# Kernel optimization log

Hardware: AMD Instinct MI355X
Metric: run time of the kernel (lower is better)

Reference implementation:

```python
import jax, jax.numpy as jnp
import numpy as np

B, NB, NS, C, HID, NP, NH = 8, 2048, 1024, 768, 3072, 1024, 6
HD = C // NH


def _ln(x, w, b):
    mu = x.mean(-1, keepdims=True)
    var = ((x - mu) ** 2).mean(-1, keepdims=True)
    return (x - mu) / jnp.sqrt(var + 1e-5) * w + b


def _gelu(z):
    return jax.nn.gelu(z, approximate=False)  # torch nn.GELU default = exact erf


def setup_inputs() -> dict:
    key = jax.random.key(0)
    ks = jax.random.split(key, 16)
    p = lambda i, shape: (jax.random.normal(ks[i], shape, jnp.float32) * 0.02)
    inp = {
        'x_b': jax.random.normal(ks[0], (B, NB, C), jnp.float32),
        'x_s': jax.random.normal(ks[1], (B, NS, C), jnp.float32),
        # token_types[0,0]=0 -> KV is computed (no stale cache), as on the first call
        'token_types': jax.random.randint(ks[2], (B, NS), 0, 2, jnp.int32).at[0, 0].set(0),
        'base_idxs': jax.random.randint(ks[3], (B, NP), -3, NB).astype(jnp.int32),
        'ln1_w': jnp.ones(C, jnp.float32), 'ln1_b': jnp.zeros(C, jnp.float32),
        'ln2_w': jnp.ones(C, jnp.float32), 'ln2_b': jnp.zeros(C, jnp.float32),
        'ln3_w': jnp.ones(C, jnp.float32), 'ln3_b': jnp.zeros(C, jnp.float32),
        'Wq': p(4, (C, C)), 'Wkv': p(5, (C, 2 * C)),
        'es_w1': p(6, (C, HID)), 'es_b1': jnp.zeros(HID, jnp.float32),
        'es_w2': p(7, (HID, C)), 'es_b2': jnp.zeros(C, jnp.float32),
        'el_w1': p(8, (C, HID)), 'el_b1': jnp.zeros(HID, jnp.float32),
        'el_w2': p(9, (HID, C)), 'el_b2': jnp.zeros(C, jnp.float32),
        'mlp_w1': p(10, (C, 4 * C)), 'mlp_b1': jnp.zeros(4 * C, jnp.float32),
        'mlp_w2': p(11, (4 * C, C)), 'mlp_b2': jnp.zeros(C, jnp.float32),
    }
    return inp


def reference(x_b, x_s, token_types, base_idxs,
              ln1_w, ln1_b, ln2_w, ln2_b, ln3_w, ln3_b,
              Wq, Wkv, es_w1, es_b1, es_w2, es_b2,
              el_w1, el_b1, el_w2, el_b2,
              mlp_w1, mlp_b1, mlp_w2, mlp_b2):
    Bn, Ns, Cd = x_s.shape
    # --- norm1/norm2 + cross-attention (q from x_s, kv from x_b) ---
    xs_n = _ln(x_s, ln1_w, ln1_b)
    xb_n = _ln(x_b, ln2_w, ln2_b)
    q = (xs_n @ Wq).reshape(Bn, Ns, NH, HD).transpose(0, 2, 1, 3)          # (B,H,Ns,hd)
    kv = (xb_n @ Wkv).reshape(Bn, -1, 2, NH, HD).transpose(2, 0, 3, 1, 4)  # (2,B,H,Nb,hd)
    k_, v_ = kv[0], kv[1]
    attn = jax.nn.softmax(jnp.einsum('bhqd,bhkd->bhqk', q, k_) * (HD ** -0.5), axis=-1)
    ctx = jnp.einsum('bhqk,bhkd->bhqd', attn, v_).transpose(0, 2, 1, 3).reshape(Bn, Ns, Cd)
    # --- 2-expert MoE MLP routed by token_types (0 -> expert_s, 1 -> expert_l) ---
    out_s = _gelu(ctx @ es_w1 + es_b1) @ es_w2 + es_b2
    out_l = _gelu(ctx @ el_w1 + el_b1) @ el_w2 + el_b2
    tt = token_types[..., None]
    moe = jnp.where(tt == 0, out_s, 0.0) + jnp.where(tt == 1, out_l, 0.0)
    x = x_s + moe
    # --- residual MLP ---
    x = x + (_gelu(_ln(x, ln3_w, ln3_b) @ mlp_w1 + mlp_b1) @ mlp_w2 + mlp_b2)
    x_norm = x / jnp.maximum(jnp.linalg.norm(x, axis=-1, keepdims=True), 1e-12)
    # --- masked-token kernel (vectorized over batch, masking replaces gather) ---
    nh = base_idxs.shape[1] // 2
    ids = base_idxs[:, :nh]
    mask = ids >= 0                                        # (B,nh)
    idc = jnp.where(mask, ids, 0)
    tokens = jnp.take_along_axis(x_b, idc[:, :, None], axis=1) * mask[..., None]
    sc = jnp.einsum('bic,bjc->bij', tokens, tokens) / jnp.sqrt(jnp.float32(Cd))
    kbias = jnp.where(mask, 0.0, -1e9)[:, None, :]
    aw = jax.nn.softmax(sc + kbias, axis=-1)
    agg = jnp.einsum('bij,bjc->bic', aw, tokens)
    cnt = mask.sum(-1)
    ksum = (agg * mask[..., None]).sum(1) / jnp.maximum(cnt, 1)[:, None]
    kn = ksum / jnp.maximum(jnp.linalg.norm(ksum, axis=-1, keepdims=True), 1e-12)
    has = (cnt > 0)[:, None]
    kernel = jnp.where(has, kn, 0.0)                        # (B,C)
    pos = jnp.where(has, (jnp.einsum('bnc,bc->bn', x_norm, kernel) + 1.0) / 2.0, 0.0)
    # --- top-k selection with data-dependent valid_k and straight-through binarize ---
    kk = Ns // 8
    topv, topi = jax.lax.top_k(pos, kk)
    cnt65 = (pos > 0.65).sum(-1)
    vk = jnp.minimum(kk, jnp.maximum(kk - 10, cnt65))
    keep = jnp.arange(kk)[None, :] < vk[:, None]
    vals = topv * keep
    sel = vals[:, :, None] * jax.nn.one_hot(topi, Ns, dtype=x.dtype)
    binary = (sel > 0.0).astype(x.dtype)
    sel = sel + jax.lax.stop_gradient(binary - sel)
    return sel, topi, pos, x, kernel[:, None, :]
```

## Files before the change

### kernel.cpp

```cpp
#include <hip/hip_runtime.h>
#include <hip/hip_bf16.h>
#include <math.h>

#define B_   8
#define NB_  2048
#define NS_  1024
#define Cc_  768
#define HID_ 3072
#define NP_  1024
#define NH_  6
#define HD_  128

__device__ __forceinline__ float gelu_exact(float v) {
  return 0.5f * v * (1.0f + erff(v * 0.7071067811865476f));
}

__device__ __forceinline__ void split3(float v, unsigned short& h,
                                       unsigned short& m, unsigned short& l) {
  unsigned hb = __float_as_uint(v) & 0xffff0000u;
  float r1 = v - __uint_as_float(hb);
  unsigned mb = __float_as_uint(r1) & 0xffff0000u;
  float r2 = r1 - __uint_as_float(mb);
  unsigned lb = __float_as_uint(r2) & 0xffff0000u;
  h = (unsigned short)(hb >> 16);
  m = (unsigned short)(mb >> 16);
  l = (unsigned short)(lb >> 16);
}

typedef short bf16x8 __attribute__((ext_vector_type(8)));
typedef float f32x4 __attribute__((ext_vector_type(4)));

#define BLOCK_REDUCE_ADD(red, tid)                                              \
  for (int off_ = 128; off_; off_ >>= 1) {                                      \
    if ((tid) < off_) red[(tid)] += red[(tid) + off_];                          \
    __syncthreads();                                                            \
  }

__global__ __launch_bounds__(256) void ln_split(
    const float* __restrict__ x, unsigned short* __restrict__ y,
    const float* __restrict__ w, const float* __restrict__ b) {
  __shared__ float red[256];
  int row = blockIdx.x, tid = threadIdx.x;
  const float* xr = x + (size_t)row * Cc_;
  float v0 = xr[tid], v1 = xr[tid + 256], v2 = xr[tid + 512];
  red[tid] = v0 + v1 + v2;
  __syncthreads();
  BLOCK_REDUCE_ADD(red, tid);
  float mu = red[0] / (float)Cc_;
  __syncthreads();
  float d0 = v0 - mu, d1 = v1 - mu, d2 = v2 - mu;
  red[tid] = d0 * d0 + d1 * d1 + d2 * d2;
  __syncthreads();
  BLOCK_REDUCE_ADD(red, tid);
  float var = red[0] / (float)Cc_;
  float rs = 1.0f / sqrtf(var + 1e-5f);
  unsigned short* yr = y + (size_t)row * 2304;
  float vals[3] = {d0 * rs * w[tid] + b[tid],
                   d1 * rs * w[tid + 256] + b[tid + 256],
                   d2 * rs * w[tid + 512] + b[tid + 512]};
#pragma unroll
  for (int t = 0; t < 3; ++t) {
    int c = tid + (t << 8);
    unsigned short h16, m16, l16;
    split3(vals[t], h16, m16, l16);
    yr[c] = h16; yr[768 + c] = m16; yr[1536 + c] = l16;
  }
}

__global__ __launch_bounds__(256) void split_kernel(
    const float* __restrict__ x, unsigned short* __restrict__ y) {
  size_t idx = (size_t)blockIdx.x * 256 + threadIdx.x;
  int c = (int)(idx % Cc_);
  int row = (int)(idx / Cc_);
  unsigned short h16, m16, l16;
  split3(x[idx], h16, m16, l16);
  unsigned short* yr = y + (size_t)row * 2304;
  yr[c] = h16; yr[768 + c] = m16; yr[1536 + c] = l16;
}

__global__ __launch_bounds__(256) void rownorm_kernel(
    const float* __restrict__ x, float* __restrict__ y) {
  __shared__ float red[256];
  int row = blockIdx.x, tid = threadIdx.x;
  const float* xr = x + (size_t)row * Cc_;
  float* yr = y + (size_t)row * Cc_;
  float v0 = xr[tid], v1 = xr[tid + 256], v2 = xr[tid + 512];
  red[tid] = v0 * v0 + v1 * v1 + v2 * v2;
  __syncthreads();
  BLOCK_REDUCE_ADD(red, tid);
  float den = fmaxf(sqrtf(red[0]), 1e-12f);
  yr[tid]       = v0 / den;
  yr[tid + 256] = v1 / den;
  yr[tid + 512] = v2 / den;
}

__global__ __launch_bounds__(256) void wconv(
    const float* __restrict__ W, unsigned short* __restrict__ out,
    int K, int N, int ldw, int ncol0) {
  int k = blockIdx.x * 256 + threadIdx.x;
  int n = blockIdx.y;
  float v = W[(size_t)k * ldw + ncol0 + n];
  unsigned short h16, m16, l16;
  split3(v, h16, m16, l16);
  size_t base = (size_t)n * 3 * K;
  out[base + k] = h16;
  out[base + K + k] = m16;
  out[base + 2 * K + k] = l16;
}

template <int EPI, bool AGATHER, bool MDEV, bool SWZ>
__global__ __launch_bounds__(256) void mgemm(
    const unsigned short* __restrict__ Ap, const unsigned short* __restrict__ Bp,
    float* __restrict__ Cf, unsigned short* __restrict__ Cs,
    const float* __restrict__ bias,
    const int* __restrict__ perm, const int* __restrict__ mdev,
    int M, int N, int K, int ldc, int Kout, int nsplit,
    long azs, long bzs, long zstride, float scale) {
  __shared__ unsigned short As[2][8192];
  __shared__ unsigned short Bs[2][8192];
  int z = blockIdx.z;
  int bx, by;
  if (SWZ) {
    int gx = gridDim.x;
    int id = blockIdx.y * gx + blockIdx.x;
    int per = (gx * gridDim.y) >> 3;
    int nid = (id & 7) * per + (id >> 3);
    bx = nid % gx; by = nid / gx;
  } else {
    bx = blockIdx.x; by = blockIdx.y;
  }
  int Me = MDEV ? mdev[0] : M;
  int m0 = by * 128, n0 = bx * 128;
  if (MDEV && m0 >= Me) return;
  const unsigned short* ApB = Ap + (size_t)z * azs;
  const unsigned short* BpB = Bp + (size_t)z * bzs;
  int tid = threadIdx.x;
  int lane = tid & 63, w = tid >> 6;
  int wr = w >> 1, wc = w & 1;
  int K3 = 3 * K;
  int tps = K >> 6;
  int KT = 6 * tps;
  int span = KT / nsplit;
  int zr = z % nsplit;
  int tt0 = zr * span, tt1 = tt0 + span;

  const unsigned short* agp[4];
  const unsigned short* bgp[4];
  int wswz[4];
#pragma unroll
  for (int p = 0; p < 4; ++p) {
    int r = (tid >> 3) + 32 * p;
    int ma = m0 + r;
    if (MDEV) ma = min(ma, Me - 1);
    if (AGATHER) ma = perm[ma];
    agp[p] = ApB + (size_t)ma * K3 + (tid & 7) * 8;
    bgp[p] = BpB + (size_t)(n0 + r) * K3 + (tid & 7) * 8;
    wswz[p] = r * 64 + (((tid & 7) ^ (r & 7)) << 3);
  }

  f32x4 acc[4][4];
  f32x4 zero4 = {0.f, 0.f, 0.f, 0.f};
#pragma unroll
  for (int i = 0; i < 4; ++i)
#pragma unroll
    for (int j = 0; j < 4; ++j) acc[i][j] = zero4;

  int kg = lane >> 4;
  int frm[4], frn[4];
#pragma unroll
  for (int f = 0; f < 4; ++f) {
    frm[f] = wr * 64 + f * 16 + (lane & 15);
    frn[f] = wc * 64 + f * 16 + (lane & 15);
  }

  bf16x8 ra[4], rb[4];
  {
    int seg = tt0 / tps, kt = tt0 - seg * tps;
    int pa = (0x210100u >> (4 * seg)) & 0xF;
    int pb = (0x012010u >> (4 * seg)) & 0xF;
    size_t ao = (size_t)(pa * K + kt * 64);
    size_t bo = (size_t)(pb * K + kt * 64);
#pragma unroll
    for (int p = 0; p < 4; ++p) {
      ra[p] = *(const bf16x8*)(agp[p] + ao);
      rb[p] = *(const bf16x8*)(bgp[p] + bo);
    }
  }

  for (int tt = tt0; tt < tt1; ++tt) {
    int cur = tt & 1;
#pragma unroll
    for (int p = 0; p < 4; ++p) {
      *(bf16x8*)&As[cur][wswz[p]] = ra[p];
      *(bf16x8*)&Bs[cur][wswz[p]] = rb[p];
    }
    if (tt + 1 < tt1) {
      int seg = (tt + 1) / tps, kt = (tt + 1) - seg * tps;
      int pa = (0x210100u >> (4 * seg)) & 0xF;
      int pb = (0x012010u >> (4 * seg)) & 0xF;
      size_t ao = (size_t)(pa * K + kt * 64);
      size_t bo = (size_t)(pb * K + kt * 64);
#pragma unroll
      for (int p = 0; p < 4; ++p) {
        ra[p] = *(const bf16x8*)(agp[p] + ao);
        rb[p] = *(const bf16x8*)(bgp[p] + bo);
      }
    }
    asm volatile("s_waitcnt lgkmcnt(0)" ::: "memory");
    __builtin_amdgcn_s_barrier();
#pragma unroll
    for (int ks = 0; ks < 2; ++ks) {
      int ch = ks * 4 + kg;
      bf16x8 af[4], bf[4];
#pragma unroll
      for (int f = 0; f < 4; ++f) {
        int r = frm[f];
        af[f] = *(const bf16x8*)&As[cur][r * 64 + ((ch ^ (r & 7)) << 3)];
      }
#pragma unroll
      for (int f = 0; f < 4; ++f) {
        int r = frn[f];
        bf[f] = *(const bf16x8*)&Bs[cur][r * 64 + ((ch ^ (r & 7)) << 3)];
      }
#pragma unroll
      for (int i = 0; i < 4; ++i)
#pragma unroll
        for (int j = 0; j < 4; ++j)
          acc[i][j] = __builtin_amdgcn_mfma_f32_16x16x32_bf16(
              af[i], bf[j], acc[i][j], 0, 0, 0);
    }
  }

#pragma unroll
  for (int i = 0; i < 4; ++i) {
#pragma unroll
    for (int r = 0; r < 4; ++r) {
      int m = m0 + wr * 64 + i * 16 + kg * 4 + r;
      if (MDEV && m >= Me) continue;
#pragma unroll
      for (int j = 0; j < 4; ++j) {
        int n = n0 + wc * 64 + j * 16 + (lane & 15);
        float v = acc[i][j][r] * scale;
        if (EPI == 6) {
          Cf[(size_t)z * zstride + (size_t)m * ldc + n] = v;
        } else if (EPI == 7) {
          Cf[(size_t)z * zstride + (size_t)m * ldc + n] += v;
        } else if (EPI == 5) {
          float t = gelu_exact(v + bias[n]);
          unsigned short h16, m16, l16;
          split3(t, h16, m16, l16);
          size_t base = (size_t)m * 3 * Kout;
          Cs[base + n] = h16;
          Cs[base + Kout + n] = m16;
          Cs[base + 2 * Kout + n] = l16;
        }
      }
    }
  }
}

template <bool SCATTER>
__global__ __launch_bounds__(256) void combineP(
    const float* __restrict__ P0, const float* __restrict__ P1,
    const float* __restrict__ bias, const float* __restrict__ addsrc,
    const int* __restrict__ perm, const int* __restrict__ cnt,
    float* __restrict__ out) {
  int m = blockIdx.x;
  int c = threadIdx.x + (blockIdx.y << 8);
  if (SCATTER && m >= cnt[0]) return;
  int mo = SCATTER ? perm[m] : m;
  size_t pm = (size_t)m * 768 + c;
  out[(size_t)mo * 768 + c] =
      bias[c] + addsrc[(size_t)mo * 768 + c] + P0[pm] + P1[pm];
}

template <int EPI, int TRB, bool AGATHER, bool MDEV>
__global__ __launch_bounds__(256) void gemm128(
    const float* __restrict__ A, const float* __restrict__ Bm,
    float* __restrict__ Cm, const float* __restrict__ bias,
    const float* __restrict__ addsrc, const int* __restrict__ perm,
    const int* __restrict__ mdev,
    int M, int N, int K, int lda, int ldb, int ldc,
    int d1, int d2,
    long a_s1, long a_s2, long a_s3,
    long b_s1, long b_s2, long b_s3,
    long c_s1, long c_s2, long c_s3,
    float scale) {
  __shared__ float As[2][16][132];
  __shared__ float Bs[2][16][132];
  int z = blockIdx.z;
  int z1 = z / (d1 * d2);
  int rem = z - z1 * d1 * d2;
  int z2 = rem / d2, z3 = rem - z2 * d2;
  const float* Ab = A + (size_t)z1 * a_s1 + (size_t)z2 * a_s2 + (size_t)z3 * a_s3;
  const float* Bb = Bm + (size_t)z1 * b_s1 + (size_t)z2 * b_s2 + (size_t)z3 * b_s3;
  float* Cb = Cm + (size_t)z1 * c_s1 + (size_t)z2 * c_s2 + (size_t)z3 * c_s3;
  int Me = MDEV ? mdev[0] : M;
  int m0 = blockIdx.y * 128, n0 = blockIdx.x * 128;
  if (MDEV && m0 >= Me) return;
  int tid = threadIdx.x;
  int tx = tid & 15, ty = tid >> 4;
  int arow = tid >> 2, akq = tid & 3;
  int ma0 = m0 + arow, ma1 = m0 + arow + 64;
  if (MDEV) { ma0 = min(ma0, Me - 1); ma1 = min(ma1, Me - 1); }
  if (AGATHER) { ma0 = perm[ma0]; ma1 = perm[ma1]; }
  const float* Ap0 = Ab + (size_t)ma0 * lda + akq * 4;
  const float* Ap1 = Ab + (size_t)ma1 * lda + akq * 4;
  const float* Bp0;
  const float* Bp1;
  int bw_r0 = 0, bw_c0 = 0, bw_r1 = 0;
  if (TRB == 0) {
    bw_r0 = tid >> 5; bw_c0 = (tid & 31) * 4; bw_r1 = bw_r0 + 8;
    Bp0 = Bb + (size_t)bw_r0 * ldb + n0 + bw_c0;
    Bp1 = Bb + (size_t)bw_r1 * ldb + n0 + bw_c0;
  } else {
    Bp0 = Bb + (size_t)(n0 + arow) * ldb + akq * 4;
    Bp1 = Bb + (size_t)(n0 + arow + 64) * ldb + akq * 4;
  }
  float4 pa0 = *(const float4*)Ap0;
  float4 pa1 = *(const float4*)Ap1;
  float4 pb0 = *(const float4*)Bp0;
  float4 pb1 = *(const float4*)Bp1;
  float acc[8][8] = {};
  int nt = K >> 4;
  for (int t = 0; t < nt; ++t) {
    int cur = t & 1;
    As[cur][akq * 4 + 0][arow] = pa0.x; As[cur][akq * 4 + 1][arow] = pa0.y;
    As[cur][akq * 4 + 2][arow] = pa0.z; As[cur][akq * 4 + 3][arow] = pa0.w;
    As[cur][akq * 4 + 0][arow + 64] = pa1.x; As[cur][akq * 4 + 1][arow + 64] = pa1.y;
    As[cur][akq * 4 + 2][arow + 64] = pa1.z; As[cur][akq * 4 + 3][arow + 64] = pa1.w;
    if (TRB == 0) {
      *(float4*)&Bs[cur][bw_r0][bw_c0] = pb0;
      *(float4*)&Bs[cur][bw_r1][bw_c0] = pb1;
    } else {
      Bs[cur][akq * 4 + 0][arow] = pb0.x; Bs[cur][akq * 4 + 1][arow] = pb0.y;
      Bs[cur][akq * 4 + 2][arow] = pb0.z; Bs[cur][akq * 4 + 3][arow] = pb0.w;
      Bs[cur][akq * 4 + 0][arow + 64] = pb1.x; Bs[cur][akq * 4 + 1][arow + 64] = pb1.y;
      Bs[cur][akq * 4 + 2][arow + 64] = pb1.z; Bs[cur][akq * 4 + 3][arow + 64] = pb1.w;
    }
    if (t + 1 < nt) {
      int kn = (t + 1) << 4;
      pa0 = *(const float4*)&Ap0[kn];
      pa1 = *(const float4*)&Ap1[kn];
      if (TRB == 0) {
        pb0 = *(const float4*)&Bp0[(size_t)kn * ldb];
        pb1 = *(const float4*)&Bp1[(size_t)kn * ldb];
      } else {
        pb0 = *(const float4*)&Bp0[kn];
        pb1 = *(const float4*)&Bp1[kn];
      }
    }
    asm volatile("s_waitcnt lgkmcnt(0)" ::: "memory");
    __builtin_amdgcn_s_barrier();
#pragma unroll
    for (int kk = 0; kk < 16; ++kk) {
      float a[8], b[8];
      *(float4*)&a[0] = *(const float4*)&As[cur][kk][ty * 4];
      *(float4*)&a[4] = *(const float4*)&As[cur][kk][ty * 4 + 64];
      *(float4*)&b[0] = *(const float4*)&Bs[cur][kk][tx * 4];
      *(float4*)&b[4] = *(const float4*)&Bs[cur][kk][tx * 4 + 64];
#pragma unroll
      for (int i = 0; i < 8; ++i)
#pragma unroll
        for (int j = 0; j < 8; ++j)
          acc[i][j] = fmaf(a[i], b[j], acc[i][j]);
    }
  }
#pragma unroll
  for (int i = 0; i < 8; ++i) {
    int m = m0 + ((i < 4) ? (ty * 4 + i) : (64 + ty * 4 + i - 4));
    if (!MDEV || m < Me) {
      int mo = (EPI == 4) ? perm[m] : m;
      int n = n0 + tx * 4;
      float v[8];
#pragma unroll
      for (int j = 0; j < 8; ++j) {
        int nj = (j < 4) ? (n + j) : (n + 64 + j - 4);
        v[j] = acc[i][j] * scale;
        if (EPI >= 1) v[j] += bias[nj];
        if (EPI == 2) v[j] = gelu_exact(v[j]);
        if (EPI == 3 || EPI == 4) v[j] += addsrc[(size_t)mo * ldc + nj];
      }
      float* cp = &Cb[(size_t)mo * ldc + n];
      *(float4*)cp = make_float4(v[0], v[1], v[2], v[3]);
      *(float4*)(cp + 64) = make_float4(v[4], v[5], v[6], v[7]);
    }
  }
}

__global__ __launch_bounds__(256) void pv_reduce(
    const float* __restrict__ part, float* __restrict__ ctx) {
  int i = blockIdx.x * 256 + threadIdx.x;
  int n = i & 127, m = (i >> 7) & 1023, h = i >> 17;
  float s = 0.f;
#pragma unroll
  for (int ks = 0; ks < 16; ++ks)
    s += part[(size_t)(ks * 6 + h) * 131072 + m * 128 + n];
  ctx[(size_t)m * 768 + h * 128 + n] = s;
}

template <int EPT, bool MASK>
__global__ __launch_bounds__(256) void softmax_kernel(
    float* __restrict__ s, const float* __restrict__ maskf) {
  __shared__ float red[256];
  int row = blockIdx.x, tid = threadIdx.x;
  float* sr = s + (size_t)row * (EPT * 256);
  const float* mb = MASK ? (maskf + (size_t)(row / 512) * 512) : nullptr;
  float v[EPT];
  float m = -3.0e38f;
#pragma unroll
  for (int t = 0; t < EPT; ++t) {
    int j = tid + (t << 8);
    float xv = sr[j];
    if (MASK) xv += (mb[j] != 0.0f) ? 0.0f : -1e9f;
    v[t] = xv;
    m = fmaxf(m, xv);
  }
  red[tid] = m;
  __syncthreads();
  for (int off = 128; off; off >>= 1) {
    if (tid < off) red[tid] = fmaxf(red[tid], red[tid + off]);
    __syncthreads();
  }
  m = red[0];
  __syncthreads();
  float ssum = 0.f;
#pragma unroll
  for (int t = 0; t < EPT; ++t) {
    v[t] = __expf(v[t] - m);
    ssum += v[t];
  }
  red[tid] = ssum;
  __syncthreads();
  BLOCK_REDUCE_ADD(red, tid);
  float tot = red[0];
#pragma unroll
  for (int t = 0; t < EPT; ++t) sr[tid + (t << 8)] = v[t] / tot;
}

__global__ __launch_bounds__(256) void build_perm(
    const int* __restrict__ tt, int* __restrict__ perm0,
    int* __restrict__ perm1, int* __restrict__ cnt) {
  int r = blockIdx.x * 256 + threadIdx.x;
  int t = tt[r];
  if (t == 0) { int p = atomicAdd(&cnt[0], 1); perm0[p] = r; }
  else        { int p = atomicAdd(&cnt[1], 1); perm1[p] = r; }
}

__global__ __launch_bounds__(256) void gather_kernel(
    const float* __restrict__ xb, const int* __restrict__ bidx,
    float* __restrict__ tokens, float* __restrict__ maskf) {
  size_t idx = (size_t)blockIdx.x * 256 + threadIdx.x;
  int c = (int)(idx % Cc_);
  int i = (int)((idx / Cc_) % 512);
  int b = (int)(idx / ((size_t)Cc_ * 512));
  int id = bidx[b * NP_ + i];
  bool m = id >= 0;
  int idc = m ? id : 0;
  tokens[idx] = m ? xb[((size_t)b * NB_ + idc) * Cc_ + c] : 0.0f;
  if (c == 0) maskf[b * 512 + i] = m ? 1.0f : 0.0f;
}

__global__ __launch_bounds__(256) void kernel_kernel(
    const float* __restrict__ agg, const float* __restrict__ maskf,
    float* __restrict__ kern, float* __restrict__ hasf) {
  __shared__ float red[256];
  __shared__ float ks[Cc_];
  __shared__ float s_cnt;
  int b = blockIdx.x, tid = threadIdx.x;
  const float* mb = maskf + b * 512;
  red[tid] = mb[tid] + mb[tid + 256];
  __syncthreads();
  BLOCK_REDUCE_ADD(red, tid);
  if (tid == 0) s_cnt = red[0];
  __syncthreads();
  float cnt = s_cnt;
  float dc = fmaxf(cnt, 1.0f);
  const float* ab = agg + (size_t)b * 512 * Cc_;
#pragma unroll
  for (int t = 0; t < 3; ++t) {
    int cc = tid + t * 256;
    float s = 0.f;
    for (int i = 0; i < 512; ++i) s = fmaf(ab[(size_t)i * Cc_ + cc], mb[i], s);
    ks[cc] = s / dc;
  }
  __syncthreads();
  float s2 = 0.f;
#pragma unroll
  for (int t = 0; t < 3; ++t) {
    float q = ks[tid + t * 256];
    s2 = fmaf(q, q, s2);
  }
  red[tid] = s2;
  __syncthreads();
  BLOCK_REDUCE_ADD(red, tid);
  float den = fmaxf(sqrtf(red[0]), 1e-12f);
  bool has = cnt > 0.5f;
#pragma unroll
  for (int t = 0; t < 3; ++t) {
    int cc = tid + t * 256;
    kern[(size_t)b * Cc_ + cc] = has ? (ks[cc] / den) : 0.0f;
  }
  if (tid == 0) hasf[b] = has ? 1.0f : 0.0f;
}

__global__ __launch_bounds__(256) void pos_kernel(
    const float* __restrict__ xnorm, const float* __restrict__ kern,
    const float* __restrict__ hasf, float* __restrict__ pos) {
  __shared__ float red[256];
  int row = blockIdx.x, tid = threadIdx.x;
  int b = row >> 10;
  const float* xr = xnorm + (size_t)row * Cc_;
  const float* kr = kern + (size_t)b * Cc_;
  float s = xr[tid] * kr[tid];
  s = fmaf(xr[tid + 256], kr[tid + 256], s);
  s = fmaf(xr[tid + 512], kr[tid + 512], s);
  red[tid] = s;
  __syncthreads();
  BLOCK_REDUCE_ADD(red, tid);
  if (tid == 0) pos[row] = (hasf[b] > 0.5f) ? (red[0] + 1.0f) * 0.5f : 0.0f;
}

__global__ __launch_bounds__(256) void topk_kernel(
    const float* __restrict__ pos, float* __restrict__ sel,
    float* __restrict__ topi) {
  __shared__ float vals[NS_];
  __shared__ float rv[256];
  __shared__ int ri[256];
  __shared__ int s_vk;
  int b = blockIdx.x, tid = threadIdx.x;
  const float* pr = pos + (size_t)b * NS_;
  int c65 = 0;
#pragma unroll
  for (int t = 0; t < 4; ++t) {
    float v = pr[tid + (t << 8)];
    vals[tid + (t << 8)] = v;
    if (v > 0.65f) ++c65;
  }
  ri[tid] = c65;
  __syncthreads();
  for (int off = 128; off; off >>= 1) {
    if (tid < off) ri[tid] += ri[tid + off];
    __syncthreads();
  }
  if (tid == 0) {
    int vk = ri[0] > 118 ? ri[0] : 118;
    s_vk = vk > 128 ? 128 : vk;
  }
  __syncthreads();
  int vk = s_vk;
  for (int r = 0; r < 128; ++r) {
    float bv = -3.0e38f;
    int bi = 0x7fffffff;
#pragma unroll
    for (int t = 0; t < 4; ++t) {
      int i = tid + (t << 8);
      float v = vals[i];
      if (v > bv) { bv = v; bi = i; }
    }
    rv[tid] = bv; ri[tid] = bi;
    __syncthreads();
    for (int off = 128; off; off >>= 1) {
      if (tid < off) {
        float ov = rv[tid + off]; int oi = ri[tid + off];
        if (ov > rv[tid] || (ov == rv[tid] && oi < ri[tid])) {
          rv[tid] = ov; ri[tid] = oi;
        }
      }
      __syncthreads();
    }
    if (tid == 0) {
      int wi = ri[0]; float wv = rv[0];
      topi[(size_t)b * 128 + r] = (float)wi;
      if (r < vk && wv > 0.0f) sel[((size_t)b * 128 + r) * NS_ + wi] = 1.0f;
      vals[wi] = -3.0e38f;
    }
    __syncthreads();
  }
}

extern "C" void kernel_launch(void* const* d_in, const int* in_sizes, int n_in,
                              void* d_out, int out_size, void* d_ws, size_t ws_size,
                              hipStream_t stream) {
  (void)in_sizes; (void)n_in; (void)out_size; (void)ws_size;
  const float* x_b = (const float*)d_in[0];
  const float* x_s = (const float*)d_in[1];
  const int* token_types = (const int*)d_in[2];
  const int* base_idxs = (const int*)d_in[3];
  const float* ln1_w = (const float*)d_in[4];
  const float* ln1_b = (const float*)d_in[5];
  const float* ln2_w = (const float*)d_in[6];
  const float* ln2_b = (const float*)d_in[7];
  const float* ln3_w = (const float*)d_in[8];
  const float* ln3_b = (const float*)d_in[9];
  const float* Wq = (const float*)d_in[10];
  const float* Wkv = (const float*)d_in[11];
  const float* es_w1 = (const float*)d_in[12];
  const float* es_b1 = (const float*)d_in[13];
  const float* es_w2 = (const float*)d_in[14];
  const float* es_b2 = (const float*)d_in[15];
  const float* el_w1 = (const float*)d_in[16];
  const float* el_b1 = (const float*)d_in[17];
  const float* el_w2 = (const float*)d_in[18];
  const float* el_b2 = (const float*)d_in[19];
  const float* mlp_w1 = (const float*)d_in[20];
  const float* mlp_b1 = (const float*)d_in[21];
  const float* mlp_w2 = (const float*)d_in[22];
  const float* mlp_b2 = (const float*)d_in[23];

  float* out = (float*)d_out;
  float* sel_out  = out;
  float* topi_out = out + 1048576;
  float* pos_out  = out + 1049600;
  float* x_out    = out + 1057792;
  float* kern_out = out + 7349248;

  float* w = (float*)d_ws;
  float* kv_f = w;
  float* q_f  = w + 25165824;
  float* scores = w + 31457280;
  float* part   = w + 44040192;
  float* ctxf   = w + 56623104;
  unsigned short* xbnp = (unsigned short*)(w + 31457280);
  unsigned short* xsnp = (unsigned short*)(w + 50331648);
  unsigned short* wqp  = (unsigned short*)(w + 59768832);
  unsigned short* wkvp = (unsigned short*)(w + 60653568);
  unsigned short* ctxp = (unsigned short*)(w + 6291456);
  unsigned short* wb   = (unsigned short*)(w + 15728640);
  unsigned short* hp   = (unsigned short*)(w + 36962304);
  float* P0 = w;
  const long ZS = 55836672;
  float* P1 = w + ZS;
  float* xn     = w + 6291456;
  float* tokens = w + 12582912;
  float* aw     = w + 15728640;
  float* agg    = w + 17825792;
  float* small  = w + 62914560;
  float* maskf  = small;
  float* hasf   = small + 4096;
  int* cnt      = (int*)(small + 4104);
  int* perm0    = (int*)(small + 4106);
  int* perm1    = (int*)(small + 12298);

  unsigned short* esw1h[2] = {wb + 0,        wb + 3538944};
  unsigned short* elw1h[2] = {wb + 7077888,  wb + 10616832};
  unsigned short* mlw1h[2] = {wb + 14155776, wb + 17694720};
  unsigned short* esw2h[2] = {wb + 21233664, wb + 24772608};
  unsigned short* elw2h[2] = {wb + 28311552, wb + 31850496};
  unsigned short* mlw2h[2] = {wb + 35389440, wb + 38928384};

  const long NSC = (long)NS_ * Cc_;
  const long NB2C = (long)NB_ * 2 * Cc_;
  const long SNB = (long)NS_ * NB_;
  const float qk_scale = 0.08838834764831845f;
  const float sc_scale = 0.036084391824351615f;

  hipMemsetAsync(sel_out, 0, (size_t)1048576 * sizeof(float), stream);
  hipMemsetAsync(cnt, 0, 2 * sizeof(int), stream);

  ln_split<<<B_ * NS_, 256, 0, stream>>>(x_s, xsnp, ln1_w, ln1_b);
  ln_split<<<B_ * NB_, 256, 0, stream>>>(x_b, xbnp, ln2_w, ln2_b);
  build_perm<<<32, 256, 0, stream>>>(token_types, perm0, perm1, cnt);
  wconv<<<dim3(3, 768), 256, 0, stream>>>(Wq, wqp, 768, 768, 768, 0);
  wconv<<<dim3(3, 1536), 256, 0, stream>>>(Wkv, wkvp, 768, 1536, 1536, 0);
  mgemm<6, false, false, true><<<dim3(6, 64, 1), 256, 0, stream>>>(
      xsnp, wqp, q_f, nullptr, nullptr, nullptr, nullptr,
      8192, 768, 768, 768, 0, 1, 0, 0, 0, 1.0f);
  mgemm<6, false, false, true><<<dim3(12, 128, 1), 256, 0, stream>>>(
      xbnp, wkvp, kv_f, nullptr, nullptr, nullptr, nullptr,
      16384, 1536, 768, 1536, 0, 1, 0, 0, 0, 1.0f);

  for (int b = 0; b < B_; ++b) {
    const float* qb = q_f + (size_t)b * NSC;
    const float* kb = kv_f + (size_t)b * NB2C;
    const float* vb = kb + Cc_;
    gemm128<0, 1, false, false><<<dim3(16, 8, 6), 256, 0, stream>>>(
        qb, kb, scores, nullptr, nullptr, nullptr, nullptr,
        1024, 2048, 128, 768, 1536, 2048,
        1, 1, 128, 0, 0, 128, 0, 0, SNB, 0, 0, qk_scale);
    softmax_kernel<8, false><<<6 * 1024, 256, 0, stream>>>(scores, nullptr);
    gemm128<0, 0, false, false><<<dim3(1, 8, 96), 256, 0, stream>>>(
        scores, vb, part, nullptr, nullptr, nullptr, nullptr,
        1024, 128, 128, 2048, 1536, 128,
        6, 16, 0, SNB, 128, 0, 128, 128 * 1536, 0, 131072, 786432, 1.0f);
    pv_reduce<<<3072, 256, 0, stream>>>(part, ctxf + (size_t)b * NSC);
  }

  split_kernel<<<24576, 256, 0, stream>>>(ctxf, ctxp);
  for (int h = 0; h < 2; ++h) {
    wconv<<<dim3(3, 1536), 256, 0, stream>>>(es_w1, esw1h[h], 768, 1536, 3072, h * 1536);
    wconv<<<dim3(3, 1536), 256, 0, stream>>>(el_w1, elw1h[h], 768, 1536, 3072, h * 1536);
    wconv<<<dim3(3, 1536), 256, 0, stream>>>(mlp_w1, mlw1h[h], 768, 1536, 3072, h * 1536);
    wconv<<<dim3(6, 768), 256, 0, stream>>>(es_w2 + (size_t)h * 1536 * 768, esw2h[h], 1536, 768, 768, 0);
    wconv<<<dim3(6, 768), 256, 0, stream>>>(el_w2 + (size_t)h * 1536 * 768, elw2h[h], 1536, 768, 768, 0);
    wconv<<<dim3(6, 768), 256, 0, stream>>>(mlp_w2 + (size_t)h * 1536 * 768, mlw2h[h], 1536, 768, 768, 0);
  }

  for (int h = 0; h < 2; ++h) {
    mgemm<5, true, true, false><<<dim3(12, 64, 1), 256, 0, stream>>>(
        ctxp, esw1h[h], nullptr, hp, es_b1 + h * 1536, perm0, cnt,
        8192, 1536, 768, 0, 1536, 1, 0, 0, 0, 1.0f);
    if (h == 0)
      mgemm<6, false, true, false><<<dim3(6, 64, 2), 256, 0, stream>>>(
          hp, esw2h[h], P0, nullptr, nullptr, nullptr, cnt,
          8192, 768, 1536, 768, 0, 2, 0, 0, ZS, 1.0f);
    else
      mgemm<7, false, true, false><<<dim3(6, 64, 2), 256, 0, stream>>>(
          hp, esw2h[h], P0, nullptr, nullptr, nullptr, cnt,
          8192, 768, 1536, 768, 0, 2, 0, 0, ZS, 1.0f);
  }
  combineP<true><<<dim3(8192, 3), 256, 0, stream>>>(
      P0, P1, es_b2, x_s, perm0, cnt, x_out);
  for (int h = 0; h < 2; ++h) {
    mgemm<5, true, true, false><<<dim3(12, 64, 1), 256, 0, stream>>>(
        ctxp, elw1h[h], nullptr, hp, el_b1 + h * 1536, perm1, cnt + 1,
        8192, 1536, 768, 0, 1536, 1, 0, 0, 0, 1.0f);
    if (h == 0)
      mgemm<6, false, true, false><<<dim3(6, 64, 2), 256, 0, stream>>>(
          hp, elw2h[h], P0, nullptr, nullptr, nullptr, cnt + 1,
          8192, 768, 1536, 768, 0, 2, 0, 0, ZS, 1.0f);
    else
      mgemm<7, false, true, false><<<dim3(6, 64, 2), 256, 0, stream>>>(
          hp, elw2h[h], P0, nullptr, nullptr, nullptr, cnt + 1,
          8192, 768, 1536, 768, 0, 2, 0, 0, ZS, 1.0f);
  }
  combineP<true><<<dim3(8192, 3), 256, 0, stream>>>(
      P0, P1, el_b2, x_s, perm1, cnt + 1, x_out);
  ln_split<<<B_ * NS_, 256, 0, stream>>>(x_out, ctxp, ln3_w, ln3_b);
  for (int h = 0; h < 2; ++h) {
    mgemm<5, false, false, true><<<dim3(12, 64, 1), 256, 0, stream>>>(
        ctxp, mlw1h[h], nullptr, hp, mlp_b1 + h * 1536, nullptr, nullptr,
        8192, 1536, 768, 0, 1536, 1, 0, 0, 0, 1.0f);
    if (h == 0)
      mgemm<6, false, false, true><<<dim3(6, 64, 2), 256, 0, stream>>>(
          hp, mlw2h[h], P0, nullptr, nullptr, nullptr, nullptr,
          8192, 768, 1536, 768, 0, 2, 0, 0, ZS, 1.0f);
    else
      mgemm<7, false, false, true><<<dim3(6, 64, 2), 256, 0, stream>>>(
          hp, mlw2h[h], P0, nullptr, nullptr, nullptr, nullptr,
          8192, 768, 1536, 768, 0, 2, 0, 0, ZS, 1.0f);
  }
  combineP<false><<<dim3(8192, 3), 256, 0, stream>>>(
      P0, P1, mlp_b2, x_out, nullptr, nullptr, x_out);

  rownorm_kernel<<<B_ * NS_, 256, 0, stream>>>(x_out, xn);
  gather_kernel<<<12288, 256, 0, stream>>>(x_b, base_idxs, tokens, maskf);
  gemm128<0, 1, false, false><<<dim3(4, 4, 8), 256, 0, stream>>>(
      tokens, tokens, aw, nullptr, nullptr, nullptr, nullptr,
      512, 512, 768, 768, 768, 512,
      1, 1, 393216, 0, 0, 393216, 0, 0, 262144, 0, 0, sc_scale);
  softmax_kernel<2, true><<<8 * 512, 256, 0, stream>>>(aw, maskf);
  gemm128<0, 0, false, false><<<dim3(6, 4, 8), 256, 0, stream>>>(
      aw, tokens, agg, nullptr, nullptr, nullptr, nullptr,
      512, 768, 512, 512, 768, 768,
      1, 1, 262144, 0, 0, 393216, 0, 0, 393216, 0, 0, 1.0f);
  kernel_kernel<<<8, 256, 0, stream>>>(agg, maskf, kern_out, hasf);
  pos_kernel<<<B_ * NS_, 256, 0, stream>>>(xn, kern_out, hasf, pos_out);
  topk_kernel<<<8, 256, 0, stream>>>(pos_out, sel_out, topi_out);
}
```

Baseline: 3.335 ms.

## Batch weight conversions into one launch, bitonic top-k, reciprocal softmax normalize

Replaces twelve separate weight-split launches with a single 3D-grid kernel that selects matrix and half by blockIdx.z, cutting launch overhead at the cost of many early-exit blocks. Rewrites the top-k kernel from 128 sequential argmax reductions into one shared-memory bitonic sort of 1024 (value, index) pairs, which cuts the number of barrier-heavy rounds. Softmax now multiplies by a reciprocal instead of dividing per element. Output offsets in the fused conversion rely on the workspace layout matching the previous per-buffer pointers.

```diff
diff --git a/kernel.cpp b/kernel.cpp
--- a/kernel.cpp
+++ b/kernel.cpp
@@ -106,6 +106,40 @@
   out[base + k] = h16;
   out[base + K + k] = m16;
   out[base + 2 * K + k] = l16;
+}
+
+__global__ __launch_bounds__(256) void wconv12(
+    const float* __restrict__ w1a, const float* __restrict__ w1b,
+    const float* __restrict__ w1c, const float* __restrict__ w2a,
+    const float* __restrict__ w2b, const float* __restrict__ w2c,
+    unsigned short* __restrict__ wb) {
+  int z = blockIdx.z;
+  int k = blockIdx.x * 256 + threadIdx.x;
+  int n = blockIdx.y;
+  const float* W;
+  int K, ldw, ncol0;
+  size_t out_off;
+  if (z < 6) {
+    K = 768; ldw = 3072;
+    int m = z >> 1, h = z & 1;
+    W = (m == 0) ? w1a : ((m == 1) ? w1b : w1c);
+    ncol0 = h * 1536;
+    out_off = (size_t)m * 7077888 + (size_t)h * 3538944;
+    if (k >= 768) return;
+  } else {
+    K = 1536; ldw = 768; ncol0 = 0;
+    int m = (z - 6) >> 1, h = z & 1;
+    W = ((m == 0) ? w2a : ((m == 1) ? w2b : w2c)) + (size_t)h * 1536 * 768;
+    out_off = 21233664 + (size_t)m * 7077888 + (size_t)h * 3538944;
+    if (n >= 768) return;
+  }
+  float v = W[(size_t)k * ldw + ncol0 + n];
+  unsigned short h16, m16, l16;
+  split3(v, h16, m16, l16);
+  size_t base = out_off + (size_t)n * 3 * K;
+  wb[base + k] = h16;
+  wb[base + K + k] = m16;
+  wb[base + 2 * K + k] = l16;
 }
 
 template <int EPI, bool AGATHER, bool MDEV, bool SWZ>
@@ -433,9 +467,9 @@
   red[tid] = ssum;
   __syncthreads();
   BLOCK_REDUCE_ADD(red, tid);
-  float tot = red[0];
-#pragma unroll
-  for (int t = 0; t < EPT; ++t) sr[tid + (t << 8)] = v[t] / tot;
+  float inv = 1.0f / red[0];
+#pragma unroll
+  for (int t = 0; t < EPT; ++t) sr[tid + (t << 8)] = v[t] * inv;
 }
 
 __global__ __launch_bounds__(256) void build_perm(
@@ -524,58 +558,56 @@
 __global__ __launch_bounds__(256) void topk_kernel(
     const float* __restrict__ pos, float* __restrict__ sel,
     float* __restrict__ topi) {
-  __shared__ float vals[NS_];
-  __shared__ float rv[256];
-  __shared__ int ri[256];
+  __shared__ float sv[NS_];
+  __shared__ int si[NS_];
+  __shared__ int red[256];
   __shared__ int s_vk;
   int b = blockIdx.x, tid = threadIdx.x;
   const float* pr = pos + (size_t)b * NS_;
   int c65 = 0;
 #pragma unroll
   for (int t = 0; t < 4; ++t) {
-    float v = pr[tid + (t << 8)];
-    vals[tid + (t << 8)] = v;
+    int i = tid + (t << 8);
+    float v = pr[i];
+    sv[i] = v; si[i] = i;
     if (v > 0.65f) ++c65;
   }
-  ri[tid] = c65;
+  red[tid] = c65;
   __syncthreads();
   for (int off = 128; off; off >>= 1) {
-    if (tid < off) ri[tid] += ri[tid + off];
+    if (tid < off) red[tid] += red[tid + off];
     __syncthreads();
   }
   if (tid == 0) {
-    int vk = ri[0] > 118 ? ri[0] : 118;
+    int vk = red[0] > 118 ? red[0] : 118;
     s_vk = vk > 128 ? 128 : vk;
   }
-  __syncthreads();
-  int vk = s_vk;
-  for (int r = 0; r < 128; ++r) {
-    float bv = -3.0e38f;
-    int bi = 0x7fffffff;
-#pragma unroll
-    for (int t = 0; t < 4; ++t) {
-      int i = tid + (t << 8);
-      float v = vals[i];
-      if (v > bv) { bv = v; bi = i; }
-    }
-    rv[tid] = bv; ri[tid] = bi;
-    __syncthreads();
-    for (int off = 128; off; off >>= 1) {
-      if (tid < off) {
-        float ov = rv[tid + off]; int oi = ri[tid + off];
-        if (ov > rv[tid] || (ov == rv[tid] && oi < ri[tid])) {
-          rv[tid] = ov; ri[tid] = oi;
+  for (int k = 2; k <= NS_; k <<= 1) {
+    for (int j = k >> 1; j > 0; j >>= 1) {
+      __syncthreads();
+#pragma unroll
+      for (int t = 0; t < 4; ++t) {
+        int i = tid + (t << 8);
+        int l = i ^ j;
+        if (l > i) {
+          bool up = ((i & k) == 0);
+          float vi = sv[i], vl = sv[l];
+          int ii = si[i], il = si[l];
+          bool gt = (vi < vl) || (vi == vl && ii > il);
+          if (up == gt) {
+            sv[i] = vl; sv[l] = vi;
+            si[i] = il; si[l] = ii;
+          }
         }
       }
-      __syncthreads();
-    }
-    if (tid == 0) {
-      int wi = ri[0]; float wv = rv[0];
-      topi[(size_t)b * 128 + r] = (float)wi;
-      if (r < vk && wv > 0.0f) sel[((size_t)b * 128 + r) * NS_ + wi] = 1.0f;
-      vals[wi] = -3.0e38f;
-    }
-    __syncthreads();
+    }
+  }
+  __syncthreads();
+  if (tid < 128) {
+    int wi = si[tid];
+    float wv = sv[tid];
+    topi[(size_t)b * 128 + tid] = (float)wi;
+    if (tid < s_vk && wv > 0.0f) sel[((size_t)b * 128 + tid) * NS_ + wi] = 1.0f;
   }
 }
 
@@ -687,14 +719,8 @@
   }
 
   split_kernel<<<24576, 256, 0, stream>>>(ctxf, ctxp);
-  for (int h = 0; h < 2; ++h) {
-    wconv<<<dim3(3, 1536), 256, 0, stream>>>(es_w1, esw1h[h], 768, 1536, 3072, h * 1536);
-    wconv<<<dim3(3, 1536), 256, 0, stream>>>(el_w1, elw1h[h], 768, 1536, 3072, h * 1536);
-    wconv<<<dim3(3, 1536), 256, 0, stream>>>(mlp_w1, mlw1h[h], 768, 1536, 3072, h * 1536);
-    wconv<<<dim3(6, 768), 256, 0, stream>>>(es_w2 + (size_t)h * 1536 * 768, esw2h[h], 1536, 768, 768, 0);
-    wconv<<<dim3(6, 768), 256, 0, stream>>>(el_w2 + (size_t)h * 1536 * 768, elw2h[h], 1536, 768, 768, 0);
-    wconv<<<dim3(6, 768), 256, 0, stream>>>(mlp_w2 + (size_t)h * 1536 * 768, mlw2h[h], 1536, 768, 768, 0);
-  }
+  wconv12<<<dim3(6, 1536, 12), 256, 0, stream>>>(
+      es_w1, el_w1, mlp_w1, es_w2, el_w2, mlp_w2, wb);
 
   for (int h = 0; h < 2; ++h) {
     mgemm<5, true, true, false><<<dim3(12, 64, 1), 256, 0, stream>>>(
```

Measured after the change: 3.199 ms. -4.1%, faster.
